# Performance work log

Hardware: AMD Instinct MI355X
Metric: run time of the kernel (lower is better)

The kernel has to match this reference:

```python
import jax, jax.numpy as jnp
import numpy as np

LAYERS = 3
DILATION = 2
RES_NORM = 1.0 / np.sqrt(2.0).astype(np.float32)
NEG_SLOPE = 0.2
T, B, D = 256, 128, 1024


def setup_inputs() -> dict:
    key = jax.random.key(0)
    k0, k1, k2, k3, k4 = jax.random.split(key, 5)
    s = 1.0 / np.sqrt(D)  # torch GRUCell default init bound
    x = jax.random.normal(k0, (1, T, B, D), dtype=jnp.float32)
    W_ih = jax.random.uniform(k1, (LAYERS, 3 * D, D), jnp.float32, -s, s)
    W_hh = jax.random.uniform(k2, (LAYERS, 3 * D, D), jnp.float32, -s, s)
    b_ih = jax.random.uniform(k3, (LAYERS, 3 * D), jnp.float32, -s, s)
    b_hh = jax.random.uniform(k4, (LAYERS, 3 * D), jnp.float32, -s, s)
    return {"x": x, "W_ih": W_ih, "W_hh": W_hh, "b_ih": b_ih, "b_hh": b_hh}


def _gru_cell(x, h, W_ih, W_hh, b_ih, b_hh):
    # torch.nn.GRUCell math
    gi = x @ W_ih.T + b_ih  # [B, 3D]
    gh = h @ W_hh.T + b_hh  # [B, 3D]
    i_r, i_z, i_n = jnp.split(gi, 3, axis=-1)
    h_r, h_z, h_n = jnp.split(gh, 3, axis=-1)
    r = jax.nn.sigmoid(i_r + h_r)
    z = jax.nn.sigmoid(i_z + h_z)
    n = jnp.tanh(i_n + r * h_n)
    return (1.0 - z) * n + z * h


def reference(x, W_ih, W_hh, b_ih, b_hh):
    xs = x[0]  # squeeze(0) -> [T, B, D]
    b, d = xs.shape[1], xs.shape[2]
    # dilated hidden buffers: layer l keeps DILATION**l past hiddens (init None -> zeros)
    bufs0 = tuple(jnp.zeros((DILATION ** l, b, d), xs.dtype) for l in range(LAYERS))

    def step(bufs, x_t):
        h_in = x_t
        new_bufs = []
        for l in range(LAYERS):
            h_out = _gru_cell(h_in, bufs[l][0], W_ih[l], W_hh[l], b_ih[l], b_hh[l])
            # append h_out, pop oldest (roll buffer)
            new_bufs.append(jnp.concatenate([bufs[l][1:], h_out[None]], axis=0))
            # layers > 1 -> dilated residual + LeakyReLU(0.2), scaled by 1/sqrt(2)
            h_in = jax.nn.leaky_relu((h_out + h_in) * RES_NORM, negative_slope=NEG_SLOPE)
        return tuple(new_bufs), h_in

    _, outs = jax.lax.scan(step, bufs0, xs)  # outs: [T, B, D]
    return outs[None]  # unsqueeze(0) -> [1, T, B, D]
```

## Files before the change

kernel.cpp:

```cpp
#include <hip/hip_runtime.h>
#include <hip/hip_bf16.h>

#define TT 256
#define D 1024
#define BD (128 * 1024)
#define NWPL 85
#define NWG 256
#define NUSED 255
#define ROWLEN 1048

typedef __attribute__((ext_vector_type(8))) short bf16x8;
typedef __attribute__((ext_vector_type(4))) float f32x4;

__device__ __forceinline__ unsigned short f2bf(float f) {
    __hip_bfloat16 h = __float2bfloat16(f);
    return *reinterpret_cast<unsigned short*>(&h);
}
__device__ __forceinline__ float bf2f(unsigned short u) {
    unsigned v = (unsigned)u << 16;
    return __builtin_bit_cast(float, v);
}

__global__ __launch_bounds__(256) void cvt_f32_bf16(const float* __restrict__ in,
                                                    unsigned short* __restrict__ out, int n) {
    int i = (blockIdx.x * 256 + threadIdx.x) * 8;
    if (i + 8 <= n) {
        float4 a = *(const float4*)(in + i);
        float4 b = *(const float4*)(in + i + 4);
        unsigned short t[8] = { f2bf(a.x), f2bf(a.y), f2bf(a.z), f2bf(a.w),
                                f2bf(b.x), f2bf(b.y), f2bf(b.z), f2bf(b.w) };
        *(uint4*)(out + i) = *(const uint4*)t;
    }
}

__global__ __launch_bounds__(256, 1) void dgru_dataflow(
    const unsigned short* __restrict__ xbf,
    const float* __restrict__ Wih, const float* __restrict__ Whh,
    const float* __restrict__ bih, const float* __restrict__ bhh,
    unsigned short* __restrict__ ring_bf,
    float* __restrict__ ring_f,
    unsigned short* __restrict__ hin_ring,
    float* __restrict__ out,
    unsigned* __restrict__ prog)
{
    __shared__ unsigned short wlds[78 * ROWLEN];

    const int grp = blockIdx.x & 7;
    const int p = 32 * grp + (blockIdx.x >> 3);
    if (p >= NUSED) return;
    const int layer = p / NWPL;
    const int u     = p % NWPL;
    const int ncols = (u < 4) ? 13 : 12;
    const int c0    = u * 12 + (u < 4 ? u : 4);

    {
        const float* w0 = Wih + (size_t)layer * 3 * D * D;
        const float* w1 = Whh + (size_t)layer * 3 * D * D;
        const int nrows = 6 * ncols;
        for (int rid = 0; rid < nrows; ++rid) {
            int m   = rid / (3 * ncols);
            int rem = rid - m * 3 * ncols;
            int g   = rem / ncols;
            int c   = rem - g * ncols;
            const float* src = (m ? w1 : w0) + ((size_t)g * D + c0 + c) * D + threadIdx.x * 4;
            float4 v = *(const float4*)src;
            ushort4 o = { f2bf(v.x), f2bf(v.y), f2bf(v.z), f2bf(v.w) };
            *(ushort4*)&wlds[rid * ROWLEN + threadIdx.x * 4] = o;
        }
        __syncthreads();
    }

    const int tid  = threadIdx.x;
    const int wave = tid >> 6;
    const int lane = tid & 63;
    const int r15  = lane & 15;
    const int kq   = lane >> 4;
    const int kq8  = kq * 8;
    const int c_cl = (r15 < ncols) ? r15 : (ncols - 1);
    const bool cvalid = r15 < ncols;
    const int col  = c0 + c_cl;

    const float bi2 = bih[layer * 3 * D + 2 * D + col];
    const float bh2 = bhh[layer * 3 * D + 2 * D + col];
    const float bs0 = bih[layer * 3 * D + col] + bhh[layer * 3 * D + col];
    const float bs1 = bih[layer * 3 * D + D + col] + bhh[layer * 3 * D + D + col];

    const unsigned short* bp[6];
    #pragma unroll
    for (int mg = 0; mg < 6; ++mg) bp[mg] = wlds + (mg * ncols + c_cl) * ROWLEN;

    const int arow_off0 = (wave * 32 + r15) * D;
    const int arow_off1 = (wave * 32 + 16 + r15) * D;

    const int dil = 1 << layer;

    unsigned* pr0 = prog;
    unsigned* pr1 = prog + 128;
    unsigned* pr2 = prog + 256;
    unsigned* myflag = prog + layer * 128 + u;

    const int j2 = (lane < 21) ? lane + 64 : lane;

    for (int t = 0; t < TT; ++t) {
        int th1, th2, th3; unsigned *a1, *a2, *a3;
        if (layer == 0)      { a1 = pr0; th1 = t;     a2 = pr1; th2 = t - 30; a3 = pr2; th3 = 0;      }
        else if (layer == 1) { a1 = pr0; th1 = t + 1; a2 = pr1; th2 = t - 1;  a3 = pr2; th3 = t - 30; }
        else                 { a1 = pr1; th1 = t + 1; a2 = pr2; th2 = t - 3;  a3 = pr2; th3 = 0;      }

        if (wave == 0) {
            for (;;) {
                bool ok = true;
                if (th1 > 0) ok = ok && (int)__hip_atomic_load(a1 + lane, __ATOMIC_RELAXED, __HIP_MEMORY_SCOPE_AGENT) >= th1
                                     && (int)__hip_atomic_load(a1 + j2,   __ATOMIC_RELAXED, __HIP_MEMORY_SCOPE_AGENT) >= th1;
                if (th2 > 0) ok = ok && (int)__hip_atomic_load(a2 + lane, __ATOMIC_RELAXED, __HIP_MEMORY_SCOPE_AGENT) >= th2
                                     && (int)__hip_atomic_load(a2 + j2,   __ATOMIC_RELAXED, __HIP_MEMORY_SCOPE_AGENT) >= th2;
                if (th3 > 0) ok = ok && (int)__hip_atomic_load(a3 + lane, __ATOMIC_RELAXED, __HIP_MEMORY_SCOPE_AGENT) >= th3
                                     && (int)__hip_atomic_load(a3 + j2,   __ATOMIC_RELAXED, __HIP_MEMORY_SCOPE_AGENT) >= th3;
                if (__all(ok)) break;
                __builtin_amdgcn_s_sleep(1);
            }
            if ((t & 15) == 0)
                __builtin_amdgcn_fence(__ATOMIC_ACQUIRE, "agent");
        }
        __syncthreads();

        const unsigned short* hinb = layer ? hin_ring + (size_t)((layer - 1) * 32 + (t & 31)) * BD
                                           : xbf + (size_t)t * BD;
        const int rs = (t + 32 - dil) & 31, wsl = t & 31;
        const unsigned short* hprevb = ring_bf + (size_t)(layer * 32 + rs) * BD;
        const float*  hprevf = ring_f + (size_t)(layer * 32 + rs) * BD;
        float*        houtf  = ring_f + (size_t)(layer * 32 + wsl) * BD;
        unsigned short* houtb = ring_bf + (size_t)(layer * 32 + wsl) * BD;

        float hpv[8], rsv[8];
        #pragma unroll
        for (int rtl = 0; rtl < 2; ++rtl)
            #pragma unroll
            for (int q = 0; q < 4; ++q) {
                const int row = wave * 32 + rtl * 16 + kq * 4 + q;
                const size_t idx = (size_t)row * D + col;
                hpv[rtl * 4 + q] = hprevf[idx];
                rsv[rtl * 4 + q] = bf2f(hinb[idx]);
            }

        f32x4 acc[2][2][3] = {};
        bf16x8 A0[16], A1[16], A2[16];

#define ISSUE1(Av, KS, SL) { \
        Av[(SL) * 4 + 0] = *(const bf16x8*)(hinb   + arow_off0 + (KS) * 32 + kq8); \
        Av[(SL) * 4 + 1] = *(const bf16x8*)(hprevb + arow_off0 + (KS) * 32 + kq8); \
        Av[(SL) * 4 + 2] = *(const bf16x8*)(hinb   + arow_off1 + (KS) * 32 + kq8); \
        Av[(SL) * 4 + 3] = *(const bf16x8*)(hprevb + arow_off1 + (KS) * 32 + kq8); }
#define ISSUEG(Av, BASE) { ISSUE1(Av, (BASE) + 0, 0) ISSUE1(Av, (BASE) + 1, 1) \
                           ISSUE1(Av, (BASE) + 2, 2) ISSUE1(Av, (BASE) + 3, 3) \
                           __builtin_amdgcn_sched_barrier(0); }
#define COMPG(Av, BASE) { _Pragma("unroll") for (int kk = 0; kk < 4; ++kk) { \
        bf16x8 Bv[6]; \
        _Pragma("unroll") for (int mg = 0; mg < 6; ++mg) \
            Bv[mg] = *(const bf16x8*)(bp[mg] + ((BASE) + kk) * 32 + kq8); \
        _Pragma("unroll") for (int g = 0; g < 3; ++g) { \
            acc[0][0][g] = __builtin_amdgcn_mfma_f32_16x16x32_bf16(Av[kk * 4 + 0], Bv[g],     acc[0][0][g], 0, 0, 0); \
            acc[0][1][g] = __builtin_amdgcn_mfma_f32_16x16x32_bf16(Av[kk * 4 + 1], Bv[3 + g], acc[0][1][g], 0, 0, 0); \
            acc[1][0][g] = __builtin_amdgcn_mfma_f32_16x16x32_bf16(Av[kk * 4 + 2], Bv[g],     acc[1][0][g], 0, 0, 0); \
            acc[1][1][g] = __builtin_amdgcn_mfma_f32_16x16x32_bf16(Av[kk * 4 + 3], Bv[3 + g], acc[1][1][g], 0, 0, 0); } } \
        __builtin_amdgcn_sched_barrier(0); }

        ISSUEG(A0, 0);  ISSUEG(A1, 4);  ISSUEG(A2, 8);
        COMPG(A0, 0);   ISSUEG(A0, 12);
        COMPG(A1, 4);   ISSUEG(A1, 16);
        COMPG(A2, 8);   ISSUEG(A2, 20);
        COMPG(A0, 12);  ISSUEG(A0, 24);
        COMPG(A1, 16);  ISSUEG(A1, 28);
        COMPG(A2, 20);
        COMPG(A0, 24);
        COMPG(A1, 28);

        #pragma unroll
        for (int rtl = 0; rtl < 2; ++rtl) {
            #pragma unroll
            for (int q = 0; q < 4; ++q) {
                const int row = wave * 32 + rtl * 16 + kq * 4 + q;
                const size_t idx = (size_t)row * D + col;
                float xr = acc[rtl][0][0][q] + acc[rtl][1][0][q] + bs0;
                float xz = acc[rtl][0][1][q] + acc[rtl][1][1][q] + bs1;
                float rg = 1.f / (1.f + __expf(-xr));
                float zg = 1.f / (1.f + __expf(-xz));
                float ng = tanhf(acc[rtl][0][2][q] + bi2 + rg * (acc[rtl][1][2][q] + bh2));
                float hp = hpv[rtl * 4 + q];
                float h  = (1.f - zg) * ng + zg * hp;
                float v = (h + rsv[rtl * 4 + q]) * 0.70710678f;
                float y = v > 0.f ? v : 0.2f * v;
                if (cvalid) {
                    __hip_atomic_store(&houtf[idx], h, __ATOMIC_RELAXED, __HIP_MEMORY_SCOPE_AGENT);
                    __hip_atomic_store(&houtb[idx], f2bf(h), __ATOMIC_RELAXED, __HIP_MEMORY_SCOPE_AGENT);
                    if (layer == 2) {
                        __hip_atomic_store(&out[(size_t)t * BD + idx], y, __ATOMIC_RELAXED, __HIP_MEMORY_SCOPE_AGENT);
                    } else {
                        __hip_atomic_store(&hin_ring[(size_t)(layer * 32 + (t & 31)) * BD + idx],
                                           f2bf(y), __ATOMIC_RELAXED, __HIP_MEMORY_SCOPE_AGENT);
                    }
                }
            }
        }

        __syncthreads();
        if (tid == 0) {
            __builtin_amdgcn_fence(__ATOMIC_RELEASE, "agent");
            __hip_atomic_store(myflag, (unsigned)(t + 1), __ATOMIC_RELAXED, __HIP_MEMORY_SCOPE_AGENT);
        }
    }
}

extern "C" void kernel_launch(void* const* d_in, const int* in_sizes, int n_in,
                              void* d_out, int out_size, void* d_ws, size_t ws_size,
                              hipStream_t stream) {
    const float* x   = (const float*)d_in[0];
    const float* Wih = (const float*)d_in[1];
    const float* Whh = (const float*)d_in[2];
    const float* bih = (const float*)d_in[3];
    const float* bhh = (const float*)d_in[4];
    float* out = (float*)d_out;

    char* ws = (char*)d_ws;
    size_t off = 0;
    auto alloc = [&](size_t bytes) -> void* {
        void* p = ws + off;
        off += (bytes + 255) & ~(size_t)255;
        return p;
    };

    const int NX = TT * BD;
    unsigned short* xbf = (unsigned short*)alloc((size_t)NX * 2);

    size_t zstart = off;
    unsigned short* ring_bf  = (unsigned short*)alloc((size_t)96 * BD * 2);
    float*          ring_f   = (float*)alloc((size_t)96 * BD * 4);
    unsigned short* hin_ring = (unsigned short*)alloc((size_t)64 * BD * 2);
    unsigned*       prog     = (unsigned*)alloc(2048);
    size_t zbytes = off - zstart;

    cvt_f32_bf16<<<NX / 8 / 256, 256, 0, stream>>>(x, xbf, NX);
    hipMemsetAsync(ws + zstart, 0, zbytes, stream);

    dgru_dataflow<<<NWG, 256, 0, stream>>>(
        xbf, Wih, Whh, bih, bhh,
        ring_bf, ring_f, hin_ring, out,
        prog);
}
```

Before: 5.744 ms.

## Halve workgroups per layer, keep W_hh in LDS and stream W_ih from global bf16

Reorganises the persistent dataflow GRU so each layer uses 43 workgroups with 24 output columns each, instead of 85 workgroups with 12-13 columns. Only the recurrent W_hh slice stays in LDS; W_ih is pre-converted to bf16 in a separate kernel and read from global/L2 on every step. This doubles the MFMA work per activation load and shrinks the flag polling set. The cost is fewer active CUs and extra global weight traffic on the critical path. It also adds an explicit vmcnt wait before the barrier that publishes each step's flag.

```diff
diff --git a/kernel.cpp b/kernel.cpp
--- a/kernel.cpp
+++ b/kernel.cpp
@@ -4,9 +4,8 @@
 #define TT 256
 #define D 1024
 #define BD (128 * 1024)
-#define NWPL 85
-#define NWG 256
-#define NUSED 255
+#define NSL 43
+#define NWG (3 * NSL)
 #define ROWLEN 1048
 
 typedef __attribute__((ext_vector_type(8))) short bf16x8;
@@ -33,9 +32,15 @@
     }
 }
 
-__global__ __launch_bounds__(256, 1) void dgru_dataflow(
+#define SB __builtin_amdgcn_sched_barrier(0)
+#define AGLD(p) __hip_atomic_load((p), __ATOMIC_RELAXED, __HIP_MEMORY_SCOPE_AGENT)
+#define AGST(p, v) __hip_atomic_store((p), (v), __ATOMIC_RELAXED, __HIP_MEMORY_SCOPE_AGENT)
+#define MF(a, b, c) __builtin_amdgcn_mfma_f32_16x16x32_bf16(a, b, c, 0, 0, 0)
+
+__global__ __launch_bounds__(256, 1) void dgru_hybrid(
     const unsigned short* __restrict__ xbf,
-    const float* __restrict__ Wih, const float* __restrict__ Whh,
+    const unsigned short* __restrict__ Wih_bf,
+    const float* __restrict__ Whh,
     const float* __restrict__ bih, const float* __restrict__ bhh,
     unsigned short* __restrict__ ring_bf,
     float* __restrict__ ring_f,
@@ -43,26 +48,21 @@
     float* __restrict__ out,
     unsigned* __restrict__ prog)
 {
-    __shared__ unsigned short wlds[78 * ROWLEN];
-
-    const int grp = blockIdx.x & 7;
-    const int p = 32 * grp + (blockIdx.x >> 3);
-    if (p >= NUSED) return;
-    const int layer = p / NWPL;
-    const int u     = p % NWPL;
-    const int ncols = (u < 4) ? 13 : 12;
-    const int c0    = u * 12 + (u < 4 ? u : 4);
+    __shared__ unsigned short wlds[72 * ROWLEN];
+
+    const int p = blockIdx.x;
+    const int layer = p / NSL;
+    const int u     = p % NSL;
+    const int ncols = (u < 42) ? 24 : 16;
+    const int c0    = u * 24;
 
     {
-        const float* w0 = Wih + (size_t)layer * 3 * D * D;
         const float* w1 = Whh + (size_t)layer * 3 * D * D;
-        const int nrows = 6 * ncols;
+        const int nrows = 3 * ncols;
         for (int rid = 0; rid < nrows; ++rid) {
-            int m   = rid / (3 * ncols);
-            int rem = rid - m * 3 * ncols;
-            int g   = rem / ncols;
-            int c   = rem - g * ncols;
-            const float* src = (m ? w1 : w0) + ((size_t)g * D + c0 + c) * D + threadIdx.x * 4;
+            int g = rid / ncols;
+            int c = rid - g * ncols;
+            const float* src = w1 + ((size_t)g * D + c0 + c) * D + threadIdx.x * 4;
             float4 v = *(const float4*)src;
             ushort4 o = { f2bf(v.x), f2bf(v.y), f2bf(v.z), f2bf(v.w) };
             *(ushort4*)&wlds[rid * ROWLEN + threadIdx.x * 4] = o;
@@ -76,30 +76,46 @@
     const int r15  = lane & 15;
     const int kq   = lane >> 4;
     const int kq8  = kq * 8;
-    const int c_cl = (r15 < ncols) ? r15 : (ncols - 1);
-    const bool cvalid = r15 < ncols;
-    const int col  = c0 + c_cl;
-
-    const float bi2 = bih[layer * 3 * D + 2 * D + col];
-    const float bh2 = bhh[layer * 3 * D + 2 * D + col];
-    const float bs0 = bih[layer * 3 * D + col] + bhh[layer * 3 * D + col];
-    const float bs1 = bih[layer * 3 * D + D + col] + bhh[layer * 3 * D + D + col];
-
-    const unsigned short* bp[6];
+
+    int  cc[2];  bool cvalid[2];  int col[2];
     #pragma unroll
-    for (int mg = 0; mg < 6; ++mg) bp[mg] = wlds + (mg * ncols + c_cl) * ROWLEN;
-
-    const int arow_off0 = (wave * 32 + r15) * D;
-    const int arow_off1 = (wave * 32 + 16 + r15) * D;
+    for (int ct = 0; ct < 2; ++ct) {
+        int c = ct * 16 + r15;
+        cvalid[ct] = c < ncols;
+        cc[ct] = cvalid[ct] ? c : (ncols - 1);
+        col[ct] = c0 + cc[ct];
+    }
+
+    float bs0[2], bs1[2], bi2c[2], bh2c[2];
+    #pragma unroll
+    for (int ct = 0; ct < 2; ++ct) {
+        bs0[ct]  = bih[layer * 3 * D + col[ct]] + bhh[layer * 3 * D + col[ct]];
+        bs1[ct]  = bih[layer * 3 * D + D + col[ct]] + bhh[layer * 3 * D + D + col[ct]];
+        bi2c[ct] = bih[layer * 3 * D + 2 * D + col[ct]];
+        bh2c[ct] = bhh[layer * 3 * D + 2 * D + col[ct]];
+    }
+
+    const unsigned short* bpL[3][2];
+    const unsigned short* bpS[3][2];
+    const unsigned short* Wih_l = Wih_bf + (size_t)layer * 3 * D * D;
+    #pragma unroll
+    for (int g = 0; g < 3; ++g)
+        #pragma unroll
+        for (int ct = 0; ct < 2; ++ct) {
+            bpL[g][ct] = wlds + (size_t)(g * ncols + cc[ct]) * ROWLEN + kq8;
+            bpS[g][ct] = Wih_l + ((size_t)g * D + col[ct]) * D + kq8;
+        }
+
+    const int arow_off0 = (wave * 32 + r15) * D + kq8;
+    const int arow_off1 = arow_off0 + 16 * D;
 
     const int dil = 1 << layer;
 
     unsigned* pr0 = prog;
-    unsigned* pr1 = prog + 128;
-    unsigned* pr2 = prog + 256;
-    unsigned* myflag = prog + layer * 128 + u;
-
-    const int j2 = (lane < 21) ? lane + 64 : lane;
+    unsigned* pr1 = prog + 64;
+    unsigned* pr2 = prog + 128;
+    unsigned* myflag = prog + layer * 64 + u;
+    const int fi = (lane < NSL) ? lane : (NSL - 1);
 
     for (int t = 0; t < TT; ++t) {
         int th1, th2, th3; unsigned *a1, *a2, *a3;
@@ -110,12 +126,9 @@
         if (wave == 0) {
             for (;;) {
                 bool ok = true;
-                if (th1 > 0) ok = ok && (int)__hip_atomic_load(a1 + lane, __ATOMIC_RELAXED, __HIP_MEMORY_SCOPE_AGENT) >= th1
-                                     && (int)__hip_atomic_load(a1 + j2,   __ATOMIC_RELAXED, __HIP_MEMORY_SCOPE_AGENT) >= th1;
-                if (th2 > 0) ok = ok && (int)__hip_atomic_load(a2 + lane, __ATOMIC_RELAXED, __HIP_MEMORY_SCOPE_AGENT) >= th2
-                                     && (int)__hip_atomic_load(a2 + j2,   __ATOMIC_RELAXED, __HIP_MEMORY_SCOPE_AGENT) >= th2;
-                if (th3 > 0) ok = ok && (int)__hip_atomic_load(a3 + lane, __ATOMIC_RELAXED, __HIP_MEMORY_SCOPE_AGENT) >= th3
-                                     && (int)__hip_atomic_load(a3 + j2,   __ATOMIC_RELAXED, __HIP_MEMORY_SCOPE_AGENT) >= th3;
+                if (th1 > 0) ok = ok && (int)AGLD(a1 + fi) >= th1;
+                if (th2 > 0) ok = ok && (int)AGLD(a2 + fi) >= th2;
+                if (th3 > 0) ok = ok && (int)AGLD(a3 + fi) >= th3;
                 if (__all(ok)) break;
                 __builtin_amdgcn_s_sleep(1);
             }
@@ -132,38 +145,45 @@
         float*        houtf  = ring_f + (size_t)(layer * 32 + wsl) * BD;
         unsigned short* houtb = ring_bf + (size_t)(layer * 32 + wsl) * BD;
 
-        float hpv[8], rsv[8];
-        #pragma unroll
-        for (int rtl = 0; rtl < 2; ++rtl)
+        float hpv[2][2][4], rsv[2][2][4];
+        #pragma unroll
+        for (int ct = 0; ct < 2; ++ct)
             #pragma unroll
-            for (int q = 0; q < 4; ++q) {
-                const int row = wave * 32 + rtl * 16 + kq * 4 + q;
-                const size_t idx = (size_t)row * D + col;
-                hpv[rtl * 4 + q] = hprevf[idx];
-                rsv[rtl * 4 + q] = bf2f(hinb[idx]);
-            }
-
-        f32x4 acc[2][2][3] = {};
+            for (int rtl = 0; rtl < 2; ++rtl)
+                #pragma unroll
+                for (int q = 0; q < 4; ++q) {
+                    const int row = wave * 32 + rtl * 16 + kq * 4 + q;
+                    const size_t idx = (size_t)row * D + col[ct];
+                    hpv[ct][rtl][q] = hprevf[idx];
+                    rsv[ct][rtl][q] = bf2f(hinb[idx]);
+                }
+
+        f32x4 acc[2][2][6] = {};
         bf16x8 A0[16], A1[16], A2[16];
 
 #define ISSUE1(Av, KS, SL) { \
-        Av[(SL) * 4 + 0] = *(const bf16x8*)(hinb   + arow_off0 + (KS) * 32 + kq8); \
-        Av[(SL) * 4 + 1] = *(const bf16x8*)(hprevb + arow_off0 + (KS) * 32 + kq8); \
-        Av[(SL) * 4 + 2] = *(const bf16x8*)(hinb   + arow_off1 + (KS) * 32 + kq8); \
-        Av[(SL) * 4 + 3] = *(const bf16x8*)(hprevb + arow_off1 + (KS) * 32 + kq8); }
+        Av[(SL) * 4 + 0] = *(const bf16x8*)(hinb   + arow_off0 + (KS) * 32); \
+        Av[(SL) * 4 + 1] = *(const bf16x8*)(hprevb + arow_off0 + (KS) * 32); \
+        Av[(SL) * 4 + 2] = *(const bf16x8*)(hinb   + arow_off1 + (KS) * 32); \
+        Av[(SL) * 4 + 3] = *(const bf16x8*)(hprevb + arow_off1 + (KS) * 32); }
 #define ISSUEG(Av, BASE) { ISSUE1(Av, (BASE) + 0, 0) ISSUE1(Av, (BASE) + 1, 1) \
                            ISSUE1(Av, (BASE) + 2, 2) ISSUE1(Av, (BASE) + 3, 3) \
-                           __builtin_amdgcn_sched_barrier(0); }
+                           SB; }
 #define COMPG(Av, BASE) { _Pragma("unroll") for (int kk = 0; kk < 4; ++kk) { \
-        bf16x8 Bv[6]; \
-        _Pragma("unroll") for (int mg = 0; mg < 6; ++mg) \
-            Bv[mg] = *(const bf16x8*)(bp[mg] + ((BASE) + kk) * 32 + kq8); \
-        _Pragma("unroll") for (int g = 0; g < 3; ++g) { \
-            acc[0][0][g] = __builtin_amdgcn_mfma_f32_16x16x32_bf16(Av[kk * 4 + 0], Bv[g],     acc[0][0][g], 0, 0, 0); \
-            acc[0][1][g] = __builtin_amdgcn_mfma_f32_16x16x32_bf16(Av[kk * 4 + 1], Bv[3 + g], acc[0][1][g], 0, 0, 0); \
-            acc[1][0][g] = __builtin_amdgcn_mfma_f32_16x16x32_bf16(Av[kk * 4 + 2], Bv[g],     acc[1][0][g], 0, 0, 0); \
-            acc[1][1][g] = __builtin_amdgcn_mfma_f32_16x16x32_bf16(Av[kk * 4 + 3], Bv[3 + g], acc[1][1][g], 0, 0, 0); } } \
-        __builtin_amdgcn_sched_barrier(0); }
+        bf16x8 WS[3][2], WL[3][2]; \
+        _Pragma("unroll") for (int g = 0; g < 3; ++g) \
+        _Pragma("unroll") for (int ct = 0; ct < 2; ++ct) { \
+            WS[g][ct] = *(const bf16x8*)(bpS[g][ct] + ((BASE) + kk) * 32); \
+            WL[g][ct] = *(const bf16x8*)(bpL[g][ct] + ((BASE) + kk) * 32); } \
+        bf16x8 h0 = Av[kk * 4 + 0], p0 = Av[kk * 4 + 1]; \
+        bf16x8 h1 = Av[kk * 4 + 2], p1 = Av[kk * 4 + 3]; \
+        _Pragma("unroll") for (int g = 0; g < 3; ++g) \
+        _Pragma("unroll") for (int ct = 0; ct < 2; ++ct) { \
+            acc[0][ct][g]     = MF(h0, WS[g][ct], acc[0][ct][g]); \
+            acc[1][ct][g]     = MF(h1, WS[g][ct], acc[1][ct][g]); \
+            acc[0][ct][3 + g] = MF(p0, WL[g][ct], acc[0][ct][3 + g]); \
+            acc[1][ct][3 + g] = MF(p1, WL[g][ct], acc[1][ct][3 + g]); } } \
+        SB; }
 
         ISSUEG(A0, 0);  ISSUEG(A1, 4);  ISSUEG(A2, 8);
         COMPG(A0, 0);   ISSUEG(A0, 12);
@@ -176,37 +196,38 @@
         COMPG(A1, 28);
 
         #pragma unroll
-        for (int rtl = 0; rtl < 2; ++rtl) {
-            #pragma unroll
-            for (int q = 0; q < 4; ++q) {
-                const int row = wave * 32 + rtl * 16 + kq * 4 + q;
-                const size_t idx = (size_t)row * D + col;
-                float xr = acc[rtl][0][0][q] + acc[rtl][1][0][q] + bs0;
-                float xz = acc[rtl][0][1][q] + acc[rtl][1][1][q] + bs1;
-                float rg = 1.f / (1.f + __expf(-xr));
-                float zg = 1.f / (1.f + __expf(-xz));
-                float ng = tanhf(acc[rtl][0][2][q] + bi2 + rg * (acc[rtl][1][2][q] + bh2));
-                float hp = hpv[rtl * 4 + q];
-                float h  = (1.f - zg) * ng + zg * hp;
-                float v = (h + rsv[rtl * 4 + q]) * 0.70710678f;
-                float y = v > 0.f ? v : 0.2f * v;
-                if (cvalid) {
-                    __hip_atomic_store(&houtf[idx], h, __ATOMIC_RELAXED, __HIP_MEMORY_SCOPE_AGENT);
-                    __hip_atomic_store(&houtb[idx], f2bf(h), __ATOMIC_RELAXED, __HIP_MEMORY_SCOPE_AGENT);
-                    if (layer == 2) {
-                        __hip_atomic_store(&out[(size_t)t * BD + idx], y, __ATOMIC_RELAXED, __HIP_MEMORY_SCOPE_AGENT);
-                    } else {
-                        __hip_atomic_store(&hin_ring[(size_t)(layer * 32 + (t & 31)) * BD + idx],
-                                           f2bf(y), __ATOMIC_RELAXED, __HIP_MEMORY_SCOPE_AGENT);
-                    }
+        for (int ct = 0; ct < 2; ++ct)
+        #pragma unroll
+        for (int rtl = 0; rtl < 2; ++rtl)
+        #pragma unroll
+        for (int q = 0; q < 4; ++q) {
+            const int row = wave * 32 + rtl * 16 + kq * 4 + q;
+            const size_t idx = (size_t)row * D + col[ct];
+            float xr = acc[rtl][ct][0][q] + acc[rtl][ct][3][q] + bs0[ct];
+            float xz = acc[rtl][ct][1][q] + acc[rtl][ct][4][q] + bs1[ct];
+            float rg = 1.f / (1.f + __expf(-xr));
+            float zg = 1.f / (1.f + __expf(-xz));
+            float ng = tanhf(acc[rtl][ct][2][q] + bi2c[ct] + rg * (acc[rtl][ct][5][q] + bh2c[ct]));
+            float hp = hpv[ct][rtl][q];
+            float h  = (1.f - zg) * ng + zg * hp;
+            float v = (h + rsv[ct][rtl][q]) * 0.70710678f;
+            float y = v > 0.f ? v : 0.2f * v;
+            if (cvalid[ct]) {
+                AGST(&houtf[idx], h);
+                AGST(&houtb[idx], f2bf(h));
+                if (layer == 2) {
+                    AGST(&out[(size_t)t * BD + idx], y);
+                } else {
+                    AGST(&hin_ring[(size_t)(layer * 32 + (t & 31)) * BD + idx], f2bf(y));
                 }
             }
         }
 
+        asm volatile("s_waitcnt vmcnt(0)");
         __syncthreads();
         if (tid == 0) {
             __builtin_amdgcn_fence(__ATOMIC_RELEASE, "agent");
-            __hip_atomic_store(myflag, (unsigned)(t + 1), __ATOMIC_RELAXED, __HIP_MEMORY_SCOPE_AGENT);
+            AGST(myflag, (unsigned)(t + 1));
         }
     }
 }
@@ -230,20 +251,23 @@
     };
 
     const int NX = TT * BD;
-    unsigned short* xbf = (unsigned short*)alloc((size_t)NX * 2);
+    const int NW = 3 * 3 * D * D;
+    unsigned short* xbf    = (unsigned short*)alloc((size_t)NX * 2);
+    unsigned short* Wih_bf = (unsigned short*)alloc((size_t)NW * 2);
 
     size_t zstart = off;
     unsigned short* ring_bf  = (unsigned short*)alloc((size_t)96 * BD * 2);
     float*          ring_f   = (float*)alloc((size_t)96 * BD * 4);
     unsigned short* hin_ring = (unsigned short*)alloc((size_t)64 * BD * 2);
-    unsigned*       prog     = (unsigned*)alloc(2048);
+    unsigned*       prog     = (unsigned*)alloc(1024);
     size_t zbytes = off - zstart;
 
     cvt_f32_bf16<<<NX / 8 / 256, 256, 0, stream>>>(x, xbf, NX);
+    cvt_f32_bf16<<<NW / 8 / 256, 256, 0, stream>>>(Wih, Wih_bf, NW);
     hipMemsetAsync(ws + zstart, 0, zbytes, stream);
 
-    dgru_dataflow<<<NWG, 256, 0, stream>>>(
-        xbf, Wih, Whh, bih, bhh,
+    dgru_hybrid<<<NWG, 256, 0, stream>>>(
+        xbf, Wih_bf, Whh, bih, bhh,
         ring_bf, ring_f, hin_ring, out,
         prog);
 }
```

New measurement: 20.20 ms. 252% more time.
